# Optimization experiments

Measured on AMD Instinct MI355X. Metric: run time of the kernel, lower is better.

The kernel has to match this reference:

```python
import jax, jax.numpy as jnp
import numpy as np

B, OBS, IMG = 16384, 256, 32
CNN_LAT, LAT, H, OUT, E = 192, 256, 256, 12, 16


def _ln(x, g, b):
    m = x.mean(-1, keepdims=True)
    v = x.var(-1, keepdims=True)
    return (x - m) / jnp.sqrt(v + 1e-5) * g + b


def _conv(x, w, b):
    y = jax.lax.conv_general_dilated(x, w, (2, 2), 'SAME',
                                     dimension_numbers=('NCHW', 'OIHW', 'NCHW'))
    return jax.nn.elu(y + b[None, :, None, None])


def setup_inputs() -> dict:
    key = jax.random.key(0)
    ks = iter(jax.random.split(key, 40))

    def lin(i, o, scale=None):
        s = (1.0 / np.sqrt(i)) if scale is None else scale
        return (jax.random.normal(next(ks), (i, o), jnp.float32) * s,
                jnp.zeros((o,), jnp.float32))

    def elin(i, o, scale=None):
        s = (1.0 / np.sqrt(i)) if scale is None else scale
        return (jax.random.normal(next(ks), (E, i, o), jnp.float32) * s,
                jnp.zeros((E, o), jnp.float32))

    inp = {}
    inp['proprio'] = jax.random.normal(next(ks), (B, OBS), jnp.float32)
    inp['camera'] = jax.random.normal(next(ks), (B, 1, IMG, IMG), jnp.float32)
    # proprioception encoder: 256 -> 128 -> 64, then LayerNorm(64)
    inp['enc_w1'], inp['enc_b1'] = lin(OBS, 128)
    inp['enc_w2'], inp['enc_b2'] = lin(128, 64)
    inp['enc_ln_g'] = jnp.ones((64,), jnp.float32)
    inp['enc_ln_b'] = jnp.zeros((64,), jnp.float32)
    # CNN: 1->16 s2, 16->32 s2, flatten 32*8*8=2048 -> 192, then LayerNorm(192)
    inp['conv1_w'] = jax.random.normal(next(ks), (16, 1, 3, 3), jnp.float32) / np.sqrt(9)
    inp['conv1_b'] = jnp.zeros((16,), jnp.float32)
    inp['conv2_w'] = jax.random.normal(next(ks), (32, 16, 3, 3), jnp.float32) / np.sqrt(16 * 9)
    inp['conv2_b'] = jnp.zeros((32,), jnp.float32)
    inp['cnn_lin_w'], inp['cnn_lin_b'] = lin(32 * 8 * 8, CNN_LAT)
    inp['cnn_ln_g'] = jnp.ones((CNN_LAT,), jnp.float32)
    inp['cnn_ln_b'] = jnp.zeros((CNN_LAT,), jnp.float32)
    # router: 256 -> 128 -> 64 -> 16 (last layer gain 0.01)
    inp['router_w1'], inp['router_b1'] = lin(LAT, 128)
    inp['router_w2'], inp['router_b2'] = lin(128, 64)
    inp['router_w3'], inp['router_b3'] = lin(64, E, 0.01)
    # 16 experts (stacked): 256 -> 256 -> 256 -> 256 -> 12 (last gain 0.01)
    inp['ew1'], inp['eb1'] = elin(LAT, H)
    inp['ew2'], inp['eb2'] = elin(H, H)
    inp['ew3'], inp['eb3'] = elin(H, H)
    inp['ew4'], inp['eb4'] = elin(H, OUT, 0.01)
    return inp


def reference(proprio, camera,
              enc_w1, enc_b1, enc_w2, enc_b2, enc_ln_g, enc_ln_b,
              conv1_w, conv1_b, conv2_w, conv2_b, cnn_lin_w, cnn_lin_b,
              cnn_ln_g, cnn_ln_b,
              router_w1, router_b1, router_w2, router_b2, router_w3, router_b3,
              ew1, eb1, ew2, eb2, ew3, eb3, ew4, eb4):
    # proprioception encoder + LayerNorm -> [B, 64]
    h = jax.nn.elu(proprio @ enc_w1 + enc_b1)
    lat1d = _ln(h @ enc_w2 + enc_b2, enc_ln_g, enc_ln_b)
    # CNN encoder -> flatten -> linear -> LayerNorm -> [B, 192]
    c = _conv(camera, conv1_w, conv1_b)          # [B,16,16,16]
    c = _conv(c, conv2_w, conv2_b)               # [B,32,8,8]
    c = c.reshape(c.shape[0], -1) @ cnn_lin_w + cnn_lin_b
    lat_cnn = _ln(c, cnn_ln_g, cnn_ln_b)
    # joint latent [B, 256]
    latent = jnp.concatenate([lat1d, lat_cnn], axis=-1)
    # router gate [B, 16]
    r = jax.nn.elu(latent @ router_w1 + router_b1)
    r = jax.nn.elu(r @ router_w2 + router_b2)
    gate = jax.nn.softmax(r @ router_w3 + router_b3, axis=-1)
    # 16 experts as grouped GEMMs: [B, E, H]
    x = jax.nn.elu(jnp.einsum('bi,eij->bej', latent, ew1) + eb1)
    x = jax.nn.elu(jnp.einsum('bej,ejk->bek', x, ew2) + eb2)
    x = jax.nn.elu(jnp.einsum('bej,ejk->bek', x, ew3) + eb3)
    expert_out = jnp.einsum('bej,ejo->beo', x, ew4) + eb4  # [B,E,OUT]
    # gate-weighted combine -> [B, OUT]
    return jnp.einsum('be,beo->bo', gate, expert_out)
```

## Files before the change

kernel.cpp:

```cpp
#include <hip/hip_runtime.h>
#include <math.h>

#define BATCH 16384
#define LATD 256
#define OUTD 12
#define NE 16

typedef short bf16x8 __attribute__((ext_vector_type(8)));
typedef float f32x4 __attribute__((ext_vector_type(4)));
typedef unsigned short u16x8 __attribute__((ext_vector_type(8)));

__device__ __forceinline__ float elu_f(float x) { return x > 0.f ? x : expm1f(x); }
__device__ __forceinline__ float elu_fast(float x) { return x > 0.f ? x : (__expf(x) - 1.f); }

__device__ __forceinline__ unsigned short f2bf(float f) {
  union { float f; unsigned int u; } a; a.f = f;
  unsigned int u = a.u;
  unsigned int r = (u + 0x7FFFu + ((u >> 16) & 1u)) >> 16;
  return (unsigned short)r;
}
__device__ __forceinline__ float bf2f(unsigned short h) {
  union { unsigned int u; float f; } a; a.u = ((unsigned int)h) << 16;
  return a.f;
}

__device__ __forceinline__ int swz(int b) { return b ^ (((b >> 9) & 7) << 4); }


__global__ __launch_bounds__(256) void k_proprio(
    const float* __restrict__ P,
    const float* __restrict__ W1, const float* __restrict__ B1,
    const float* __restrict__ W2, const float* __restrict__ B2,
    const float* __restrict__ G, const float* __restrict__ Bn,
    unsigned short* __restrict__ lat16) {
  __shared__ __align__(16) float a[32][256];
  __shared__ float h[32][128];
  __shared__ float d[32][64];
  __shared__ float mrow[32], irow[32];
  const int t = threadIdx.x;
  const size_t row0 = (size_t)blockIdx.x * 32;
  {
    const float4* s = (const float4*)(P + row0 * 256);
    float4* dd = (float4*)&a[0][0];
    #pragma unroll
    for (int i = 0; i < 8; i++) dd[t + i * 256] = s[t + i * 256];
  }
  __syncthreads();
  {
    const int c = t & 127, g0 = (t >> 7) * 16;
    float acc[16];
    #pragma unroll
    for (int i = 0; i < 16; i++) acc[i] = 0.f;
    for (int k = 0; k < 256; k++) {
      const float w = W1[k * 128 + c];
      #pragma unroll
      for (int i = 0; i < 16; i++) acc[i] += a[g0 + i][k] * w;
    }
    const float bb = B1[c];
    #pragma unroll
    for (int i = 0; i < 16; i++) h[g0 + i][c] = elu_f(acc[i] + bb);
  }
  __syncthreads();
  {
    const int c = t & 63, g0 = (t >> 6) * 8;
    float acc[8];
    #pragma unroll
    for (int i = 0; i < 8; i++) acc[i] = 0.f;
    for (int k = 0; k < 128; k++) {
      const float w = W2[k * 64 + c];
      #pragma unroll
      for (int i = 0; i < 8; i++) acc[i] += h[g0 + i][k] * w;
    }
    const float bb = B2[c];
    #pragma unroll
    for (int i = 0; i < 8; i++) d[g0 + i][c] = acc[i] + bb;
  }
  __syncthreads();
  if (t < 32) {
    float m = 0.f;
    for (int j = 0; j < 64; j++) m += d[t][j];
    m *= (1.f / 64.f);
    float v = 0.f;
    for (int j = 0; j < 64; j++) { float x = d[t][j] - m; v += x * x; }
    v *= (1.f / 64.f);
    mrow[t] = m; irow[t] = 1.f / sqrtf(v + 1e-5f);
  }
  __syncthreads();
  {
    const int r = t >> 3, ch = t & 7;
    const size_t grow = row0 + r;
    const size_t rb = grow >> 7;
    const int loc = (int)(grow & 127);
    u16x8 o;
    #pragma unroll
    for (int q = 0; q < 8; q++) {
      const int c = ch * 8 + q;
      o[q] = f2bf((d[r][c] - mrow[r]) * irow[r] * G[c] + Bn[c]);
    }
    *(u16x8*)((char*)lat16 + rb * 65536 + swz(loc * 512 + ch * 16)) = o;
  }
}

__global__ __launch_bounds__(256) void k_prep(
    const float* __restrict__ ew1, const float* __restrict__ ew2, const float* __restrict__ ew3,
    const float* __restrict__ ew4, const float* __restrict__ cnn_lin_w, const float* __restrict__ C2W,
    unsigned short* __restrict__ wt1, unsigned short* __restrict__ wt2, unsigned short* __restrict__ wt3,
    unsigned short* __restrict__ w4t, unsigned short* __restrict__ cnnWb, unsigned short* __restrict__ w2g) {
  __shared__ float tile[64][65];
  const int t = threadIdx.x;
  const int bid = blockIdx.x;
  if (bid < 768) {
    const int k0 = (bid & 3) * 64, j0 = ((bid >> 2) & 3) * 64;
    const int zl = bid >> 4;
    const int layer = zl >> 4, e = zl & 15;
    const float* src = (layer == 0 ? ew1 : layer == 1 ? ew2 : ew3) + (size_t)e * 65536;
    unsigned short* dst = (layer == 0 ? wt1 : layer == 1 ? wt2 : wt3) + (size_t)e * 65536;
    for (int idx = t; idx < 4096; idx += 256) {
      const int kk = idx >> 6, jj = idx & 63;
      tile[kk][jj] = src[(size_t)(k0 + kk) * 256 + j0 + jj];
    }
    __syncthreads();
    for (int idx = t; idx < 4096; idx += 256) {
      const int jj = idx >> 6, kk = idx & 63;
      dst[(size_t)(j0 + jj) * 256 + k0 + kk] = f2bf(tile[kk][jj]);
    }
  } else if (bid < 864) {
    const int idx0 = bid - 768;
    const int k0 = (idx0 & 31) * 64, j0 = (idx0 >> 5) * 64;
    for (int idx = t; idx < 4096; idx += 256) {
      const int kk = idx >> 6, jj = idx & 63;
      tile[kk][jj] = cnn_lin_w[(size_t)(k0 + kk) * 192 + j0 + jj];
    }
    __syncthreads();
    for (int idx = t; idx < 4096; idx += 256) {
      const int jj = idx >> 6, kk = idx & 63;
      cnnWb[(size_t)(j0 + jj) * 2048 + k0 + kk] = f2bf(tile[kk][jj]);
    }
  } else if (bid < 880) {
    const int e = bid - 864, k = t;
    #pragma unroll
    for (int j = 0; j < 16; j++) {
      const float v = (j < 12) ? ew4[(size_t)e * 3072 + k * 12 + j] : 0.f;
      w4t[(size_t)e * 4096 + j * 256 + k] = f2bf(v);
    }
  } else {
    const int co = t >> 3, ci0 = t & 7;
    #pragma unroll
    for (int hh = 0; hh < 2; hh++) {
      const int ci = ci0 + hh * 8;
      #pragma unroll
      for (int tap = 0; tap < 16; tap++) {
        w2g[co * 256 + ci * 16 + tap] =
            (tap < 9) ? f2bf(C2W[co * 144 + ci * 9 + tap]) : (unsigned short)0;
      }
    }
  }
}

__global__ __launch_bounds__(256) void k_conv(
    const float* __restrict__ cam,
    const float* __restrict__ C1W, const float* __restrict__ C1B,
    const unsigned short* __restrict__ w2g, const float* __restrict__ C2B,
    unsigned short* __restrict__ flat) {
  __shared__ __align__(16) float img[32 * 36];
  __shared__ float w1s[144];
  __shared__ __align__(16) unsigned short c1[16 * 17 * 20];
  __shared__ __align__(16) unsigned short Bm[64 * 256];
  __shared__ __align__(16) unsigned short obuf[2048];
  const int t = threadIdx.x;
  const int lane = t & 63, w = t >> 6;
  const int lr = lane & 15, lg = lane >> 4;
  const size_t b = blockIdx.x;
  char* c1b = (char*)c1;
  char* bmb = (char*)Bm;
  {
    const float* ip = cam + b * 1024;
    for (int i = t; i < 1024; i += 256) img[(i >> 5) * 36 + (i & 31)] = ip[i];
    if (t < 32) *(float4*)&img[t * 36 + 32] = make_float4(0.f, 0.f, 0.f, 0.f);
    if (t < 144) w1s[t] = C1W[t];
    if (t < 80) *(ushort4*)(c1b + (t / 5) * 680 + 640 + (t % 5) * 8) = make_ushort4(0, 0, 0, 0);
  }
  __syncthreads();
  {
    const int c = t >> 4, y = t & 15;
    float acc[16];
    #pragma unroll
    for (int x = 0; x < 16; x++) acc[x] = 0.f;
    #pragma unroll
    for (int dy = 0; dy < 3; dy++) {
      const int row = 2 * y + dy;
      if (row < 32) {
        float4 f4[9];
        #pragma unroll
        for (int i = 0; i < 9; i++) f4[i] = *(const float4*)&img[row * 36 + 4 * i];
        const float* rr = (const float*)f4;
        const float wa = w1s[c * 9 + dy * 3], wb = w1s[c * 9 + dy * 3 + 1], wc = w1s[c * 9 + dy * 3 + 2];
        #pragma unroll
        for (int x = 0; x < 16; x++) acc[x] += wa * rr[2 * x] + wb * rr[2 * x + 1] + wc * rr[2 * x + 2];
      }
    }
    const float bb = C1B[c];
    #pragma unroll
    for (int p = 0; p < 4; p++) {
      ushort4 v;
      v.x = f2bf(elu_fast(acc[4 * p + 0] + bb));
      v.y = f2bf(elu_fast(acc[4 * p + 1] + bb));
      v.z = f2bf(elu_fast(acc[4 * p + 2] + bb));
      v.w = f2bf(elu_fast(acc[4 * p + 3] + bb));
      *(ushort4*)(c1b + c * 680 + y * 40 + p * 8) = v;
    }
    *(ushort4*)(c1b + c * 680 + y * 40 + 32) = make_ushort4(0, 0, 0, 0);
  }
  __syncthreads();
  {
    #pragma unroll
    for (int i = 0; i < 4; i++) {
      const int item = i * 256 + t;
      const int m = item & 63, ci = item >> 6;
      const int y = m >> 3, x = m & 7;
      unsigned int pr[3]; unsigned short th[3];
      #pragma unroll
      for (int dy = 0; dy < 3; dy++) {
        const int base = ci * 680 + (2 * y + dy) * 40 + 4 * x;
        pr[dy] = *(const unsigned int*)(c1b + base);
        th[dy] = *(const unsigned short*)(c1b + base + 4);
      }
      uint4 u0;
      u0.x = pr[0];
      u0.y = ((unsigned int)th[0]) | (((unsigned int)(pr[1] & 0xFFFFu)) << 16);
      u0.z = (pr[1] >> 16) | (((unsigned int)th[1]) << 16);
      u0.w = pr[2];
      uint4 u1;
      u1.x = (unsigned int)th[2];
      u1.y = 0; u1.z = 0; u1.w = 0;
      const int bb0 = m * 512 + ci * 32;
      *(uint4*)(bmb + swz(bb0)) = u0;
      *(uint4*)(bmb + swz(bb0 + 16)) = u1;
    }
  }
  __syncthreads();
  {
    f32x4 acc[2];
    acc[0] = (f32x4){0.f, 0.f, 0.f, 0.f};
    acc[1] = (f32x4){0.f, 0.f, 0.f, 0.f};
    const int mbase = (w * 16 + lr) * 512 + lg * 16;
    #pragma unroll
    for (int ks = 0; ks < 8; ks++) {
      const bf16x8 bfr = *(const bf16x8*)(bmb + swz(mbase + ks * 64));
      #pragma unroll
      for (int nt = 0; nt < 2; nt++) {
        const bf16x8 af = *(const bf16x8*)(w2g + (nt * 16 + lr) * 256 + ks * 32 + lg * 8);
        acc[nt] = __builtin_amdgcn_mfma_f32_16x16x32_bf16(af, bfr, acc[nt], 0, 0, 0);
      }
    }
    #pragma unroll
    for (int nt = 0; nt < 2; nt++) {
      const float4 bb = *(const float4*)(C2B + nt * 16 + 4 * lg);
      const float bv[4] = { bb.x, bb.y, bb.z, bb.w };
      #pragma unroll
      for (int q = 0; q < 4; q++) {
        const int co = nt * 16 + 4 * lg + q;
        obuf[co * 64 + w * 16 + lr] = f2bf(elu_fast(acc[nt][q] + bv[q]));
      }
    }
  }
  __syncthreads();
  *(u16x8*)(flat + b * 2048 + t * 8) = *(const u16x8*)(obuf + t * 8);
}

__global__ __launch_bounds__(256) void k_cnnlin(
    const unsigned short* __restrict__ Xc, const unsigned short* __restrict__ Wb,
    const float* __restrict__ bias, const float* __restrict__ G,
    const float* __restrict__ Bn, unsigned short* __restrict__ lat16) {
  __shared__ __align__(16) unsigned short XS[32 * 256];
  __shared__ __align__(16) float Yl[32 * 196];
  __shared__ float mrow[32], irow[32];
  char* xsb = (char*)XS;
  const int t = threadIdx.x;
  const int lane = t & 63, w = t >> 6;
  const int lr = lane & 15, lg = lane >> 4;
  const int b0 = blockIdx.x * 32;
  const int j0w = w * 48;

  f32x4 acc[3][2];
  #pragma unroll
  for (int jt = 0; jt < 3; jt++)
    #pragma unroll
    for (int mt = 0; mt < 2; mt++) acc[jt][mt] = (f32x4){0.f, 0.f, 0.f, 0.f};

  for (int kc = 0; kc < 8; kc++) {
    #pragma unroll
    for (int i = 0; i < 4; i++) {
      const int f = t + i * 256;
      const int m = f >> 5;
      const int kof = (f & 31) * 8;
      const u16x8 v = *(const u16x8*)(Xc + (size_t)(b0 + m) * 2048 + kc * 256 + kof);
      *(u16x8*)(xsb + swz(m * 512 + kof * 2)) = v;
    }
    __syncthreads();
    #pragma unroll
    for (int ks = 0; ks < 8; ks++) {
      bf16x8 af[3], bfr[2];
      #pragma unroll
      for (int jt = 0; jt < 3; jt++)
        af[jt] = *(const bf16x8*)(Wb + (size_t)(j0w + jt * 16 + lr) * 2048 + kc * 256 + ks * 32 + lg * 8);
      #pragma unroll
      for (int mt = 0; mt < 2; mt++)
        bfr[mt] = *(const bf16x8*)(xsb + swz((mt * 16 + lr) * 512 + lg * 16 + ks * 64));
      #pragma unroll
      for (int jt = 0; jt < 3; jt++)
        #pragma unroll
        for (int mt = 0; mt < 2; mt++)
          acc[jt][mt] = __builtin_amdgcn_mfma_f32_16x16x32_bf16(af[jt], bfr[mt], acc[jt][mt], 0, 0, 0);
    }
    __syncthreads();
  }
  #pragma unroll
  for (int jt = 0; jt < 3; jt++) {
    const int j0 = j0w + jt * 16 + 4 * lg;
    const float4 bb = *(const float4*)(bias + j0);
    #pragma unroll
    for (int mt = 0; mt < 2; mt++) {
      const int m = mt * 16 + lr;
      f32x4 v = acc[jt][mt];
      v[0] += bb.x; v[1] += bb.y; v[2] += bb.z; v[3] += bb.w;
      *(f32x4*)&Yl[m * 196 + j0] = v;
    }
  }
  __syncthreads();
  if (t < 32) {
    float m = 0.f;
    for (int q = 0; q < 48; q++) {
      const f32x4 v = *(const f32x4*)&Yl[t * 196 + q * 4];
      m += v[0] + v[1] + v[2] + v[3];
    }
    m *= (1.f / 192.f);
    float var = 0.f;
    for (int q = 0; q < 48; q++) {
      const f32x4 v = *(const f32x4*)&Yl[t * 196 + q * 4];
      #pragma unroll
      for (int z = 0; z < 4; z++) { const float x = v[z] - m; var += x * x; }
    }
    var *= (1.f / 192.f);
    mrow[t] = m; irow[t] = 1.f / sqrtf(var + 1e-5f);
  }
  __syncthreads();
  {
    #pragma unroll
    for (int i = 0; i < 3; i++) {
      const int item = t + i * 256;
      const int m = item / 24, cq = item % 24;
      const float mm = mrow[m], iv = irow[m];
      u16x8 o;
      #pragma unroll
      for (int q = 0; q < 8; q++) {
        const int j = cq * 8 + q;
        o[q] = f2bf((Yl[m * 196 + j] - mm) * iv * G[j] + Bn[j]);
      }
      const size_t grow = (size_t)(b0 + m);
      const size_t rb = grow >> 7;
      const int loc = (int)(grow & 127);
      *(u16x8*)((char*)lat16 + rb * 65536 + swz(loc * 512 + 128 + cq * 16)) = o;
    }
  }
}

__global__ __launch_bounds__(256) void k_router(
    const unsigned short* __restrict__ lat16,
    const float* __restrict__ W1, const float* __restrict__ B1,
    const float* __restrict__ W2, const float* __restrict__ B2,
    const float* __restrict__ W3, const float* __restrict__ B3,
    float* __restrict__ gate) {
  __shared__ __align__(16) float a[32][256];
  __shared__ float h1[32][128];
  __shared__ float h2[32][64];
  __shared__ float lg[32][16];
  const int t = threadIdx.x;
  const size_t row0 = (size_t)blockIdx.x * 32;
  {
    #pragma unroll
    for (int i = 0; i < 4; i++) {
      const int cc = t + i * 256;
      const int r = cc >> 5, kc = cc & 31;
      const size_t grow = row0 + r;
      const size_t rb = grow >> 7;
      const int loc = (int)(grow & 127);
      const u16x8 h = *(const u16x8*)((const char*)lat16 + rb * 65536 + swz(loc * 512 + kc * 16));
      #pragma unroll
      for (int q = 0; q < 8; q++) a[r][kc * 8 + q] = bf2f(h[q]);
    }
  }
  __syncthreads();
  {
    const int c = t & 127, g0 = (t >> 7) * 16;
    float acc[16];
    #pragma unroll
    for (int i = 0; i < 16; i++) acc[i] = 0.f;
    for (int k = 0; k < 256; k++) {
      const float w = W1[k * 128 + c];
      #pragma unroll
      for (int i = 0; i < 16; i++) acc[i] += a[g0 + i][k] * w;
    }
    const float bb = B1[c];
    #pragma unroll
    for (int i = 0; i < 16; i++) h1[g0 + i][c] = elu_f(acc[i] + bb);
  }
  __syncthreads();
  {
    const int c = t & 63, g0 = (t >> 6) * 8;
    float acc[8];
    #pragma unroll
    for (int i = 0; i < 8; i++) acc[i] = 0.f;
    for (int k = 0; k < 128; k++) {
      const float w = W2[k * 64 + c];
      #pragma unroll
      for (int i = 0; i < 8; i++) acc[i] += h1[g0 + i][k] * w;
    }
    const float bb = B2[c];
    #pragma unroll
    for (int i = 0; i < 8; i++) h2[g0 + i][c] = elu_f(acc[i] + bb);
  }
  __syncthreads();
  for (int o = t; o < 512; o += 256) {
    const int r = o >> 4, c = o & 15;
    float acc = 0.f;
    for (int k = 0; k < 64; k++) acc += h2[r][k] * W3[k * 16 + c];
    lg[r][c] = acc + B3[c];
  }
  __syncthreads();
  if (t < 32) {
    float m = lg[t][0];
    for (int c = 1; c < 16; c++) m = fmaxf(m, lg[t][c]);
    float s = 0.f;
    float ex[16];
    for (int c = 0; c < 16; c++) { ex[c] = expf(lg[t][c] - m); s += ex[c]; }
    const float inv = 1.f / s;
    for (int c = 0; c < 16; c++) gate[(row0 + t) * 16 + c] = ex[c] * inv;
  }
}

__global__ __launch_bounds__(256) void k_experts(
    const unsigned short* __restrict__ lat16, const float* __restrict__ gate,
    const unsigned short* __restrict__ wt1, const unsigned short* __restrict__ wt2,
    const unsigned short* __restrict__ wt3, const unsigned short* __restrict__ w4t,
    const float* __restrict__ EB1, const float* __restrict__ EB2,
    const float* __restrict__ EB3, const float* __restrict__ EB4,
    float* __restrict__ eout, int e_base) {
  __shared__ __align__(16) unsigned short X[64 * 256];
  char* sx = (char*)X;
  const int t = threadIdx.x;
  const int lane = t & 63, w = t >> 6;
  const int lr = lane & 15, lg = lane >> 4;
  const int bid = blockIdx.x;
  const int xcd = bid & 7, l = bid >> 3;
  const int e = e_base + (l >> 5);
  const int rb = xcd * 32 + (l & 31);
  const int row0 = rb * 64;

  const float gv = gate[(size_t)(row0 + w * 16 + lr) * 16 + e];

  {
    const uint4* s = (const uint4*)(lat16 + (size_t)(rb >> 1) * 32768 + (size_t)(rb & 1) * 16384);
    uint4* dd = (uint4*)X;
    #pragma unroll
    for (int i = 0; i < 8; i++) dd[t + i * 256] = s[t + i * 256];
  }
  __syncthreads();

  const unsigned short* Wl[3] = {
    wt1 + (size_t)e * 65536, wt2 + (size_t)e * 65536, wt3 + (size_t)e * 65536 };
  const float* Bl[3] = { EB1 + e * 256, EB2 + e * 256, EB3 + e * 256 };
  const int wjb = w * 64;

  int mtb[4];
  #pragma unroll
  for (int mt = 0; mt < 4; mt++) mtb[mt] = (mt * 16 + lr) * 512 + lg * 16;

  #pragma unroll
  for (int lyr = 0; lyr < 3; lyr++) {
    const unsigned short* W = Wl[lyr];
    const float* B = Bl[lyr];
    f32x4 acc[4][4];
    #pragma unroll
    for (int jt = 0; jt < 4; jt++) {
      const float4 bb = *(const float4*)(B + wjb + jt * 16 + 4 * lg);
      #pragma unroll
      for (int mt = 0; mt < 4; mt++)
        acc[jt][mt] = (f32x4){bb.x, bb.y, bb.z, bb.w};
    }
    const size_t wlane = (size_t)(wjb + lr) * 256 + lg * 8;
    for (int ks = 0; ks < 8; ks++) {
      bf16x8 af[4], bfr[4];
      #pragma unroll
      for (int jt = 0; jt < 4; jt++)
        af[jt] = *(const bf16x8*)(W + wlane + jt * 4096 + ks * 32);
      #pragma unroll
      for (int mt = 0; mt < 4; mt++)
        bfr[mt] = *(const bf16x8*)(sx + swz(mtb[mt] + ks * 64));
      __builtin_amdgcn_s_setprio(1);
      #pragma unroll
      for (int jt = 0; jt < 4; jt++)
        #pragma unroll
        for (int mt = 0; mt < 4; mt++)
          acc[jt][mt] = __builtin_amdgcn_mfma_f32_16x16x32_bf16(af[jt], bfr[mt], acc[jt][mt], 0, 0, 0);
      __builtin_amdgcn_s_setprio(0);
    }
    __syncthreads();
    #pragma unroll
    for (int jt = 0; jt < 4; jt++) {
      const int j0 = wjb + jt * 16 + 4 * lg;
      #pragma unroll
      for (int mt = 0; mt < 4; mt++) {
        const int m = mt * 16 + lr;
        ushort4 h;
        h.x = f2bf(elu_fast(acc[jt][mt][0]));
        h.y = f2bf(elu_fast(acc[jt][mt][1]));
        h.z = f2bf(elu_fast(acc[jt][mt][2]));
        h.w = f2bf(elu_fast(acc[jt][mt][3]));
        *(ushort4*)(sx + swz(m * 512 + j0 * 2)) = h;
      }
    }
    __syncthreads();
  }

  {
    const unsigned short* W4 = w4t + (size_t)e * 4096;
    float4 b4 = make_float4(0.f, 0.f, 0.f, 0.f);
    if (lg < 3) b4 = *(const float4*)(EB4 + e * 12 + 4 * lg);
    f32x4 a4 = (f32x4){b4.x, b4.y, b4.z, b4.w};
    const size_t wl4 = (size_t)lr * 256 + lg * 8;
    const int mb = (w * 16 + lr) * 512 + lg * 16;
    #pragma unroll
    for (int ks = 0; ks < 8; ks++) {
      const bf16x8 a = *(const bf16x8*)(W4 + wl4 + ks * 32);
      const bf16x8 bv = *(const bf16x8*)(sx + swz(mb + ks * 64));
      a4 = __builtin_amdgcn_mfma_f32_16x16x32_bf16(a, bv, a4, 0, 0, 0);
    }
    const int row = row0 + w * 16 + lr;
    if (lg < 3) {
      float4 o;
      o.x = gv * a4[0];
      o.y = gv * a4[1];
      o.z = gv * a4[2];
      o.w = gv * a4[3];
      *(float4*)(eout + ((size_t)e * BATCH + row) * 12 + 4 * lg) = o;
    }
  }
}

__global__ __launch_bounds__(256) void k_reduce(
    const float* __restrict__ eout, float* __restrict__ out) {
  const int i = blockIdx.x * 256 + threadIdx.x;
  if (i < BATCH * OUTD) {
    float s = 0.f;
    #pragma unroll
    for (int e = 0; e < NE; e++) s += eout[(size_t)e * (BATCH * OUTD) + i];
    out[i] = s;
  }
}

extern "C" void kernel_launch(void* const* d_in, const int* in_sizes, int n_in,
                              void* d_out, int out_size, void* d_ws, size_t ws_size,
                              hipStream_t stream) {
  (void)in_sizes; (void)n_in; (void)out_size; (void)ws_size;
  const float* proprio   = (const float*)d_in[0];
  const float* camera    = (const float*)d_in[1];
  const float* enc_w1    = (const float*)d_in[2];
  const float* enc_b1    = (const float*)d_in[3];
  const float* enc_w2    = (const float*)d_in[4];
  const float* enc_b2    = (const float*)d_in[5];
  const float* enc_ln_g  = (const float*)d_in[6];
  const float* enc_ln_b  = (const float*)d_in[7];
  const float* conv1_w   = (const float*)d_in[8];
  const float* conv1_b   = (const float*)d_in[9];
  const float* conv2_w   = (const float*)d_in[10];
  const float* conv2_b   = (const float*)d_in[11];
  const float* cnn_lin_w = (const float*)d_in[12];
  const float* cnn_lin_b = (const float*)d_in[13];
  const float* cnn_ln_g  = (const float*)d_in[14];
  const float* cnn_ln_b  = (const float*)d_in[15];
  const float* rw1 = (const float*)d_in[16];
  const float* rb1 = (const float*)d_in[17];
  const float* rw2 = (const float*)d_in[18];
  const float* rb2 = (const float*)d_in[19];
  const float* rw3 = (const float*)d_in[20];
  const float* rb3 = (const float*)d_in[21];
  const float* ew1 = (const float*)d_in[22];
  const float* eb1 = (const float*)d_in[23];
  const float* ew2 = (const float*)d_in[24];
  const float* eb2 = (const float*)d_in[25];
  const float* ew3 = (const float*)d_in[26];
  const float* eb3 = (const float*)d_in[27];
  const float* ew4 = (const float*)d_in[28];
  const float* eb4 = (const float*)d_in[29];
  float* out = (float*)d_out;

  unsigned short* lat16 = (unsigned short*)d_ws;
  float* gate = (float*)(lat16 + (size_t)BATCH * 256);
  unsigned short* wt1 = (unsigned short*)(gate + (size_t)BATCH * NE);
  unsigned short* wt2 = wt1 + (size_t)NE * 65536;
  unsigned short* wt3 = wt2 + (size_t)NE * 65536;
  unsigned short* w4t = wt3 + (size_t)NE * 65536;
  unsigned short* cnnWb = w4t + (size_t)NE * 4096;
  unsigned short* w2g = cnnWb + (size_t)192 * 2048;
  unsigned short* region = w2g + (size_t)32 * 256;
  unsigned short* convflat = region;
  float* eout = (float*)region;

  k_prep<<<dim3(881), dim3(256), 0, stream>>>(ew1, ew2, ew3, ew4, cnn_lin_w, conv2_w,
                                              wt1, wt2, wt3, w4t, cnnWb, w2g);
  k_proprio<<<dim3(512), dim3(256), 0, stream>>>(proprio, enc_w1, enc_b1, enc_w2, enc_b2,
                                                 enc_ln_g, enc_ln_b, lat16);
  k_conv<<<dim3(16384), dim3(256), 0, stream>>>(camera, conv1_w, conv1_b, w2g, conv2_b, convflat);
  k_cnnlin<<<dim3(512), dim3(256), 0, stream>>>(convflat, cnnWb, cnn_lin_b,
                                                cnn_ln_g, cnn_ln_b, lat16);
  k_router<<<dim3(512), dim3(256), 0, stream>>>(lat16, rw1, rb1, rw2, rb2, rw3, rb3, gate);
  k_experts<<<dim3(2048), dim3(256), 0, stream>>>(lat16, gate, wt1, wt2, wt3, w4t,
                                                  eb1, eb2, eb3, eb4, eout, 0);
  k_experts<<<dim3(2048), dim3(256), 0, stream>>>(lat16, gate, wt1, wt2, wt3, w4t,
                                                  eb1, eb2, eb3, eb4, eout, 8);
  k_reduce<<<dim3(768), dim3(256), 0, stream>>>(eout, out);
}
```

Baseline: 560.6 us.

## Store conv2 output spatial-major and permute cnn_lin weight rows to match

The conv kernel now writes conv2 results straight from MFMA registers to global memory in a spatial-major [m][co] layout. This drops the obuf shared-memory staging buffer and its final barrier. The weight-prep kernel permutes the cnn_lin_w rows to match the new flatten order, so the math stays equivalent. The image tile pitch shrinks from 36 to 34 floats, with float2 loads, and the im2col loop mapping is reordered. The direct global stores are 8-byte writes spread across rows instead of fully coalesced 16-byte writes, which may cost some store efficiency.

```diff
diff --git a/kernel.cpp b/kernel.cpp
--- a/kernel.cpp
+++ b/kernel.cpp
@@ -129,7 +129,9 @@
     const int k0 = (idx0 & 31) * 64, j0 = (idx0 >> 5) * 64;
     for (int idx = t; idx < 4096; idx += 256) {
       const int kk = idx >> 6, jj = idx & 63;
-      tile[kk][jj] = cnn_lin_w[(size_t)(k0 + kk) * 192 + j0 + jj];
+      const int knew = k0 + kk;
+      const int kold = (knew & 31) * 64 + (knew >> 5);
+      tile[kk][jj] = cnn_lin_w[(size_t)kold * 192 + j0 + jj];
     }
     __syncthreads();
     for (int idx = t; idx < 4096; idx += 256) {
@@ -162,11 +164,10 @@
     const float* __restrict__ C1W, const float* __restrict__ C1B,
     const unsigned short* __restrict__ w2g, const float* __restrict__ C2B,
     unsigned short* __restrict__ flat) {
-  __shared__ __align__(16) float img[32 * 36];
+  __shared__ __align__(16) float img[32 * 34];
   __shared__ float w1s[144];
   __shared__ __align__(16) unsigned short c1[16 * 17 * 20];
   __shared__ __align__(16) unsigned short Bm[64 * 256];
-  __shared__ __align__(16) unsigned short obuf[2048];
   const int t = threadIdx.x;
   const int lane = t & 63, w = t >> 6;
   const int lr = lane & 15, lg = lane >> 4;
@@ -175,8 +176,8 @@
   char* bmb = (char*)Bm;
   {
     const float* ip = cam + b * 1024;
-    for (int i = t; i < 1024; i += 256) img[(i >> 5) * 36 + (i & 31)] = ip[i];
-    if (t < 32) *(float4*)&img[t * 36 + 32] = make_float4(0.f, 0.f, 0.f, 0.f);
+    for (int i = t; i < 1024; i += 256) img[(i >> 5) * 34 + (i & 31)] = ip[i];
+    if (t < 64) img[(t & 31) * 34 + 32 + (t >> 5)] = 0.f;
     if (t < 144) w1s[t] = C1W[t];
     if (t < 80) *(ushort4*)(c1b + (t / 5) * 680 + 640 + (t % 5) * 8) = make_ushort4(0, 0, 0, 0);
   }
@@ -190,13 +191,12 @@
     for (int dy = 0; dy < 3; dy++) {
       const int row = 2 * y + dy;
       if (row < 32) {
-        float4 f4[9];
+        float2 f[17];
         #pragma unroll
-        for (int i = 0; i < 9; i++) f4[i] = *(const float4*)&img[row * 36 + 4 * i];
-        const float* rr = (const float*)f4;
+        for (int i = 0; i < 17; i++) f[i] = *(const float2*)&img[row * 34 + 2 * i];
         const float wa = w1s[c * 9 + dy * 3], wb = w1s[c * 9 + dy * 3 + 1], wc = w1s[c * 9 + dy * 3 + 2];
         #pragma unroll
-        for (int x = 0; x < 16; x++) acc[x] += wa * rr[2 * x] + wb * rr[2 * x + 1] + wc * rr[2 * x + 2];
+        for (int x = 0; x < 16; x++) acc[x] += wa * f[x].x + wb * f[x].y + wc * f[x + 1].x;
       }
     }
     const float bb = C1B[c];
@@ -213,10 +213,11 @@
   }
   __syncthreads();
   {
-    #pragma unroll
-    for (int i = 0; i < 4; i++) {
-      const int item = i * 256 + t;
-      const int m = item & 63, ci = item >> 6;
+    const int ci = t & 15;
+    const int mloc = t >> 4;
+    #pragma unroll
+    for (int p = 0; p < 4; p++) {
+      const int m = p * 16 + mloc;
       const int y = m >> 3, x = m & 7;
       unsigned int pr[3]; unsigned short th[3];
       #pragma unroll
@@ -253,19 +254,18 @@
         acc[nt] = __builtin_amdgcn_mfma_f32_16x16x32_bf16(af, bfr, acc[nt], 0, 0, 0);
       }
     }
+    const int m = w * 16 + lr;
     #pragma unroll
     for (int nt = 0; nt < 2; nt++) {
       const float4 bb = *(const float4*)(C2B + nt * 16 + 4 * lg);
-      const float bv[4] = { bb.x, bb.y, bb.z, bb.w };
-      #pragma unroll
-      for (int q = 0; q < 4; q++) {
-        const int co = nt * 16 + 4 * lg + q;
-        obuf[co * 64 + w * 16 + lr] = f2bf(elu_fast(acc[nt][q] + bv[q]));
-      }
-    }
-  }
-  __syncthreads();
-  *(u16x8*)(flat + b * 2048 + t * 8) = *(const u16x8*)(obuf + t * 8);
+      ushort4 v;
+      v.x = f2bf(elu_fast(acc[nt][0] + bb.x));
+      v.y = f2bf(elu_fast(acc[nt][1] + bb.y));
+      v.z = f2bf(elu_fast(acc[nt][2] + bb.z));
+      v.w = f2bf(elu_fast(acc[nt][3] + bb.w));
+      *(ushort4*)(flat + b * 2048 + (size_t)m * 32 + nt * 16 + 4 * lg) = v;
+    }
+  }
 }
 
 __global__ __launch_bounds__(256) void k_cnnlin(
```

After: 534.7 us. 4.6% less time.
